# Kernel optimization log

Hardware: AMD Instinct MI355X
Metric: run time of the kernel (lower is better)

Reference implementation:

```python
import jax, jax.numpy as jnp
import numpy as np

B, L, D, H, M = 2, 4096, 1024, 16, 256
DH = D // H
EPS = 1e-6
LN_EPS = 1e-5


def setup_inputs() -> dict:
    key = jax.random.key(0)
    ks = jax.random.split(key, 6)
    inp = {
        "x": jax.random.normal(ks[0], (B, L, D), jnp.float32),
        "Wq": jax.random.normal(ks[1], (D, D), jnp.float32) * (D ** -0.5),
        "Wk": jax.random.normal(ks[2], (D, D), jnp.float32) * (D ** -0.5),
        "Wv": jax.random.normal(ks[3], (D, D), jnp.float32) * (D ** -0.5),
        "Wo": jax.random.normal(ks[4], (D, D), jnp.float32) * (D ** -0.5),
        "proj": jax.random.normal(ks[5], (H, M, DH), jnp.float32),
        "ln_g": jnp.ones((D,), jnp.float32),
        "ln_b": jnp.zeros((D,), jnp.float32),
        "scale_factor": 2,
    }
    return inp


def _heads(t, W):
    b, l, _ = t.shape
    return (t @ W).reshape(b, l, H, DH).transpose(0, 2, 1, 3)  # bhld


def _favor_features(u, proj):
    # u: [B,H,L,DH] already scaled by d_head**-0.25; proj: [H,M,DH]
    dash = jnp.einsum("bhld,hmd->bhlm", u, proj)
    diag = 0.5 * jnp.sum(u * u, axis=-1, keepdims=True)  # [B,H,L,1]
    stab = jnp.max(dash, axis=-1, keepdims=True)
    return jnp.exp(dash - diag - stab) * (M ** -0.5)  # [B,H,L,M]


def reference(x, Wq, Wk, Wv, Wo, proj, ln_g, ln_b, scale_factor):
    b, l, d = x.shape
    # nearest-neighbor upsample along sequence (F.interpolate default mode)
    up = jnp.repeat(x, scale_factor, axis=1)  # [B, L*s, D]

    scale = DH ** -0.25
    q = _heads(up, Wq) * scale   # [B,H,Lq,DH]
    k = _heads(x, Wk) * scale    # [B,H,L,DH]
    v = _heads(x, Wv)            # [B,H,L,DH]

    qf = _favor_features(q, proj)  # [B,H,Lq,M]
    kf = _favor_features(k, proj)  # [B,H,L,M]

    kv = jnp.einsum("bhlm,bhld->bhmd", kf, v)          # [B,H,M,DH]
    k_sum = jnp.sum(kf, axis=2)                          # [B,H,M]
    z = 1.0 / (jnp.einsum("bhlm,bhm->bhl", qf, k_sum) + EPS)
    attn = jnp.einsum("bhlm,bhmd->bhld", qf, kv) * z[..., None]

    lq = attn.shape[2]
    y = attn.transpose(0, 2, 1, 3).reshape(b, lq, d) @ Wo
    y = jax.nn.gelu(y, approximate=False)

    mu = jnp.mean(y, axis=-1, keepdims=True)
    var = jnp.mean((y - mu) ** 2, axis=-1, keepdims=True)
    return (y - mu) * jax.lax.rsqrt(var + LN_EPS) * ln_g + ln_b
```

## Files before the change

### kernel.cpp

```cpp
#include <hip/hip_runtime.h>

static constexpr int kB  = 2;
static constexpr int kL  = 4096;
static constexpr int kD  = 1024;
static constexpr int kH  = 16;
static constexpr int kDH = 64;
static constexpr int kM  = 256;
static constexpr int kN  = kB * kL;
static constexpr float kScale    = 0.35355339059327373f;
static constexpr float kInvSqrtM = 0.0625f;
static constexpr float kEps   = 1e-6f;
static constexpr float kLnEps = 1e-5f;

typedef __attribute__((ext_vector_type(8))) short short8;
typedef __attribute__((ext_vector_type(4))) float f32x4;

__device__ __forceinline__ float bf2f(unsigned short h) {
  union { unsigned int u; float f; } c;
  c.u = ((unsigned int)h) << 16;
  return c.f;
}
__device__ __forceinline__ unsigned short f2bf(float f) {
  union { float f; unsigned int u; } c;
  c.f = f;
  unsigned int u = c.u;
  u += 0x7fffu + ((u >> 16) & 1u);
  return (unsigned short)(u >> 16);
}

__device__ __forceinline__ void gload_lds16(const unsigned short* g,
                                            unsigned short* l) {
  __builtin_amdgcn_global_load_lds(
      (const __attribute__((address_space(1))) unsigned int*)g,
      (__attribute__((address_space(3))) unsigned int*)l, 16, 0, 0);
}

__device__ __forceinline__ void xcd_swizzle(int& bx, int& by) {
  const int nwg = gridDim.x * gridDim.y;
  const int bid = blockIdx.x + gridDim.x * blockIdx.y;
  const int cpx = nwg >> 3;
  const int sb  = (bid & 7) * cpx + (bid >> 3);
  bx = sb % gridDim.x;
  by = sb / gridDim.x;
}

__global__ __launch_bounds__(256) void cast_bf16_kernel(
    const float* __restrict__ in, unsigned short* __restrict__ out)
{
  const int i = blockIdx.x * 256 + threadIdx.x;
  float4 v = ((const float4*)in)[i];
  ushort4 o;
  o.x = f2bf(v.x); o.y = f2bf(v.y); o.z = f2bf(v.z); o.w = f2bf(v.w);
  ((ushort4*)out)[i] = o;
}

__global__ __launch_bounds__(256) void transpose_cast4_kernel(
    const float* __restrict__ W0, const float* __restrict__ W1,
    const float* __restrict__ W2, const float* __restrict__ W3,
    unsigned short* __restrict__ WqkvT, unsigned short* __restrict__ WoT)
{
  __shared__ float tile[32][33];
  const int z = blockIdx.z;
  const float* W = (z == 0) ? W0 : (z == 1) ? W1 : (z == 2) ? W2 : W3;
  unsigned short* WT = (z < 3) ? (WqkvT + (size_t)z * kD * kD) : WoT;
  const int n0 = blockIdx.x * 32, k0 = blockIdx.y * 32;
  const int t = threadIdx.x, kk = t >> 5, nn = t & 31;
#pragma unroll
  for (int i = 0; i < 4; ++i)
    tile[kk + i * 8][nn] = W[(size_t)(k0 + kk + i * 8) * kD + n0 + nn];
  __syncthreads();
#pragma unroll
  for (int i = 0; i < 4; ++i)
    WT[(size_t)(n0 + kk + i * 8) * kD + k0 + nn] = f2bf(tile[nn][kk + i * 8]);
}

__global__ __launch_bounds__(256) void gemm_qk_mfma(
    const unsigned short* __restrict__ A, const unsigned short* __restrict__ BT,
    unsigned short* __restrict__ Qb, unsigned short* __restrict__ Kb)
{
  __shared__ unsigned short As[128 * 32];
  __shared__ unsigned short Bs[128 * 32];
  const int tid = threadIdx.x, lane = tid & 63, w = tid >> 6;
  const int q = lane >> 4, c = lane & 15;
  const int wr = (w >> 1) * 64, wc = (w & 1) * 64;
  int bx, by; xcd_swizzle(bx, by);
  const int row0 = by * 128, col0 = bx * 128;
  const int lrow = lane >> 2, lcol = (lane & 3) * 8;

  f32x4 acc[4][4];
#pragma unroll
  for (int i = 0; i < 4; ++i)
#pragma unroll
    for (int j = 0; j < 4; ++j) acc[i][j] = (f32x4)0.f;

  for (int k0 = 0; k0 < kD; k0 += 32) {
#pragma unroll
    for (int i = 0; i < 2; ++i) {
      const int r0 = w * 32 + i * 16;
      gload_lds16(&A[(size_t)(row0 + r0 + lrow) * kD + k0 + lcol], &As[r0 * 32]);
      gload_lds16(&BT[(size_t)(col0 + r0 + lrow) * kD + k0 + lcol], &Bs[r0 * 32]);
    }
    __syncthreads();
    short8 av[4], bv[4];
#pragma unroll
    for (int i = 0; i < 4; ++i)
      av[i] = *(const short8*)&As[(wr + i * 16 + c) * 32 + q * 8];
#pragma unroll
    for (int j = 0; j < 4; ++j)
      bv[j] = *(const short8*)&Bs[(wc + j * 16 + c) * 32 + q * 8];
#pragma unroll
    for (int i = 0; i < 4; ++i)
#pragma unroll
      for (int j = 0; j < 4; ++j)
        acc[i][j] = __builtin_amdgcn_mfma_f32_16x16x32_bf16(
            av[i], bv[j], acc[i][j], 0, 0, 0);
    __syncthreads();
  }

  unsigned short* O = (col0 < 1024) ? Qb : Kb;
  const int cl0 = col0 & 1023;
#pragma unroll
  for (int i = 0; i < 4; ++i)
#pragma unroll
    for (int j = 0; j < 4; ++j)
#pragma unroll
      for (int r = 0; r < 4; ++r) {
        const int row = row0 + wr + i * 16 + q * 4 + r;
        const int col = cl0 + wc + j * 16 + c;
        O[(size_t)row * kD + col] = f2bf(kScale * acc[i][j][r]);
      }
}

__global__ __launch_bounds__(256) void gemm_vt_mfma(
    const unsigned short* __restrict__ A, const unsigned short* __restrict__ BT,
    unsigned short* __restrict__ VT)
{
  __shared__ unsigned short As[128 * 32];
  __shared__ unsigned short Bs[128 * 32];
  const int tid = threadIdx.x, lane = tid & 63, w = tid >> 6;
  const int q = lane >> 4, c = lane & 15;
  const int wr = (w >> 1) * 64, wc = (w & 1) * 64;
  int bx, by; xcd_swizzle(bx, by);
  const int row0 = bx * 128, col0 = by * 128;
  const int lrow = lane >> 2, lcol = (lane & 3) * 8;

  f32x4 acc[4][4];
#pragma unroll
  for (int i = 0; i < 4; ++i)
#pragma unroll
    for (int j = 0; j < 4; ++j) acc[i][j] = (f32x4)0.f;

  for (int k0 = 0; k0 < kD; k0 += 32) {
#pragma unroll
    for (int i = 0; i < 2; ++i) {
      const int r0 = w * 32 + i * 16;
      gload_lds16(&A[(size_t)(row0 + r0 + lrow) * kD + k0 + lcol], &As[r0 * 32]);
      gload_lds16(&BT[(size_t)(col0 + r0 + lrow) * kD + k0 + lcol], &Bs[r0 * 32]);
    }
    __syncthreads();
    short8 av[4], bv[4];
#pragma unroll
    for (int i = 0; i < 4; ++i)
      av[i] = *(const short8*)&As[(wr + i * 16 + c) * 32 + q * 8];
#pragma unroll
    for (int j = 0; j < 4; ++j)
      bv[j] = *(const short8*)&Bs[(wc + j * 16 + c) * 32 + q * 8];
#pragma unroll
    for (int i = 0; i < 4; ++i)
#pragma unroll
      for (int j = 0; j < 4; ++j)
        acc[i][j] = __builtin_amdgcn_mfma_f32_16x16x32_bf16(
            av[i], bv[j], acc[i][j], 0, 0, 0);
    __syncthreads();
  }

#pragma unroll
  for (int i = 0; i < 4; ++i)
#pragma unroll
    for (int j = 0; j < 4; ++j)
#pragma unroll
      for (int r = 0; r < 4; ++r) {
        const int row = row0 + wr + i * 16 + q * 4 + r;
        const int col = col0 + wc + j * 16 + c;
        const int bq = col >> 12, l = col & 4095;
        const int h = row >> 6, d = row & 63;
        VT[((size_t)((bq * 16 + h) * 64 + d)) * (size_t)kL + l] =
            f2bf(acc[i][j][r]);
      }
}

__global__ __launch_bounds__(256) void gemm_wo_mfma(
    const unsigned short* __restrict__ A, const unsigned short* __restrict__ BT,
    float* __restrict__ Cout)
{
  __shared__ unsigned short As[128 * 32];
  __shared__ unsigned short Bs[128 * 32];
  const int tid = threadIdx.x, lane = tid & 63, w = tid >> 6;
  const int q = lane >> 4, c = lane & 15;
  const int wr = (w >> 1) * 64, wc = (w & 1) * 64;
  int bx, by; xcd_swizzle(bx, by);
  const int row0 = by * 128, col0 = bx * 128;
  const int lrow = lane >> 2, lcol = (lane & 3) * 8;

  f32x4 acc[4][4];
#pragma unroll
  for (int i = 0; i < 4; ++i)
#pragma unroll
    for (int j = 0; j < 4; ++j) acc[i][j] = (f32x4)0.f;

  for (int k0 = 0; k0 < kD; k0 += 32) {
#pragma unroll
    for (int i = 0; i < 2; ++i) {
      const int r0 = w * 32 + i * 16;
      gload_lds16(&A[(size_t)(row0 + r0 + lrow) * kD + k0 + lcol], &As[r0 * 32]);
      gload_lds16(&BT[(size_t)(col0 + r0 + lrow) * kD + k0 + lcol], &Bs[r0 * 32]);
    }
    __syncthreads();
    short8 av[4], bv[4];
#pragma unroll
    for (int i = 0; i < 4; ++i)
      av[i] = *(const short8*)&As[(wr + i * 16 + c) * 32 + q * 8];
#pragma unroll
    for (int j = 0; j < 4; ++j)
      bv[j] = *(const short8*)&Bs[(wc + j * 16 + c) * 32 + q * 8];
#pragma unroll
    for (int i = 0; i < 4; ++i)
#pragma unroll
      for (int j = 0; j < 4; ++j)
        acc[i][j] = __builtin_amdgcn_mfma_f32_16x16x32_bf16(
            av[i], bv[j], acc[i][j], 0, 0, 0);
    __syncthreads();
  }

#pragma unroll
  for (int i = 0; i < 4; ++i)
#pragma unroll
    for (int j = 0; j < 4; ++j)
#pragma unroll
      for (int r = 0; r < 4; ++r) {
        const int row = row0 + wr + i * 16 + q * 4 + r;
        const int col = col0 + wc + j * 16 + c;
        Cout[(size_t)row * kD + col] = acc[i][j][r];
      }
}

template <int TRANS>
__global__ __launch_bounds__(256) void favor_mfma(
    const unsigned short* __restrict__ U, const unsigned short* __restrict__ projb,
    unsigned short* __restrict__ F)
{
  __shared__ unsigned short Us[128 * 72];
  __shared__ unsigned short Ps[256 * 72];
  __shared__ float diagp[256];
  __shared__ float diag[128];
  unsigned short* Tbuf = Us;
  const int bh = blockIdx.x, b = bh >> 4, h = bh & 15;
  const int l0 = blockIdx.y * 128;
  const int tid = threadIdx.x, lane = tid & 63, w = tid >> 6;
  const int q = lane >> 4, c = lane & 15;
  const int wr = w * 32;

#pragma unroll
  for (int it = 0; it < 4; ++it) {
    int idx = it * 256 + tid;
    int row = idx >> 3, col8 = idx & 7;
    *(uint4*)&Us[row * 72 + col8 * 8] =
        *(const uint4*)&U[((size_t)(b * kL + l0 + row)) * kD + h * kDH + col8 * 8];
  }
#pragma unroll
  for (int it = 0; it < 8; ++it) {
    int idx = it * 256 + tid;
    int row = idx >> 3, col8 = idx & 7;
    *(uint4*)&Ps[row * 72 + col8 * 8] =
        *(const uint4*)&projb[((size_t)(h * kM + row)) * kDH + col8 * 8];
  }
  __syncthreads();

  {
    int row = tid & 127, half = tid >> 7;
    const unsigned short* ur = &Us[row * 72 + half * 32];
    float s = 0.f;
#pragma unroll
    for (int d8 = 0; d8 < 4; ++d8) {
      uint4 raw = *(const uint4*)&ur[d8 * 8];
      const unsigned short* us = (const unsigned short*)&raw;
#pragma unroll
      for (int j = 0; j < 8; ++j) { float v = bf2f(us[j]); s = fmaf(v, v, s); }
    }
    diagp[half * 128 + row] = s;
  }

  f32x4 acc[2][16];
#pragma unroll
  for (int i = 0; i < 2; ++i)
#pragma unroll
    for (int j = 0; j < 16; ++j) acc[i][j] = (f32x4)0.f;

#pragma unroll
  for (int ks = 0; ks < 2; ++ks) {
    short8 av[2];
#pragma unroll
    for (int i = 0; i < 2; ++i)
      av[i] = *(const short8*)&Us[(wr + i * 16 + c) * 72 + ks * 32 + q * 8];
#pragma unroll
    for (int jb = 0; jb < 2; ++jb) {
      short8 bv[8];
#pragma unroll
      for (int jl = 0; jl < 8; ++jl)
        bv[jl] = *(const short8*)&Ps[((jb * 8 + jl) * 16 + c) * 72 + ks * 32 + q * 8];
#pragma unroll
      for (int jl = 0; jl < 8; ++jl)
#pragma unroll
        for (int i = 0; i < 2; ++i)
          acc[i][jb * 8 + jl] = __builtin_amdgcn_mfma_f32_16x16x32_bf16(
              av[i], bv[jl], acc[i][jb * 8 + jl], 0, 0, 0);
    }
  }

  __syncthreads();
  if (tid < 128) diag[tid] = 0.5f * (diagp[tid] + diagp[128 + tid]);
  __syncthreads();

#pragma unroll
  for (int i = 0; i < 2; ++i)
#pragma unroll
    for (int r = 0; r < 4; ++r) {
      const int lrow = wr + i * 16 + q * 4 + r;
      float mx = -3.4e38f;
#pragma unroll
      for (int j = 0; j < 16; ++j) mx = fmaxf(mx, acc[i][j][r]);
      mx = fmaxf(mx, __shfl_xor(mx, 1, 64));
      mx = fmaxf(mx, __shfl_xor(mx, 2, 64));
      mx = fmaxf(mx, __shfl_xor(mx, 4, 64));
      mx = fmaxf(mx, __shfl_xor(mx, 8, 64));
      const float base = diag[lrow] + mx;
      if (TRANS == 0) {
        const size_t gbase = ((size_t)bh * kL + (l0 + lrow)) * kM;
#pragma unroll
        for (int j = 0; j < 16; ++j)
          F[gbase + j * 16 + c] = f2bf(__expf(acc[i][j][r] - base) * kInvSqrtM);
      } else {
#pragma unroll
        for (int j = 0; j < 16; ++j)
          acc[i][j][r] = __expf(acc[i][j][r] - base) * kInvSqrtM;
      }
    }

  if (TRANS == 1) {
#pragma unroll
    for (int mc = 0; mc < 4; ++mc) {
      __syncthreads();
#pragma unroll
      for (int jl = 0; jl < 4; ++jl) {
        const int jj = mc * 4 + jl;
#pragma unroll
        for (int i = 0; i < 2; ++i) {
          ushort4 o;
          o.x = f2bf(acc[i][jj][0]); o.y = f2bf(acc[i][jj][1]);
          o.z = f2bf(acc[i][jj][2]); o.w = f2bf(acc[i][jj][3]);
          *(ushort4*)&Tbuf[(jl * 16 + c) * 136 + wr + i * 16 + q * 4] = o;
        }
      }
      __syncthreads();
#pragma unroll
      for (int it = 0; it < 4; ++it) {
        int idx = it * 256 + tid;
        int row = idx >> 4, col8 = idx & 15;
        *(uint4*)&F[((size_t)(bh * kM + mc * 64 + row)) * (size_t)kL +
                    l0 + col8 * 8] = *(const uint4*)&Tbuf[row * 136 + col8 * 8];
      }
    }
  }
}

__global__ __launch_bounds__(256) void kv_mfma(
    const unsigned short* __restrict__ KFT, const unsigned short* __restrict__ VT,
    float* __restrict__ KVP, float* __restrict__ KSP)
{
  __shared__ unsigned short As[128 * 32];
  __shared__ unsigned short Bs[64 * 32];
  const int bh = blockIdx.x, mtile = blockIdx.y, split = blockIdx.z;
  const int tid = threadIdx.x, lane = tid & 63, w = tid >> 6;
  const int q = lane >> 4, c = lane & 15;
  const int l0 = split * 512;
  const unsigned short* Abase = KFT + ((size_t)(bh * kM + mtile * 128)) * kL + l0;
  const unsigned short* Bbase = VT + ((size_t)(bh * kDH)) * kL + l0;
  const int lrow = lane >> 2, lcol = (lane & 3) * 8;

  f32x4 acc[2][4];
#pragma unroll
  for (int i = 0; i < 2; ++i)
#pragma unroll
    for (int j = 0; j < 4; ++j) acc[i][j] = (f32x4)0.f;
  float ksr[2] = {0.f, 0.f};

  for (int k0 = 0; k0 < 512; k0 += 32) {
#pragma unroll
    for (int i = 0; i < 2; ++i) {
      const int r0 = w * 32 + i * 16;
      gload_lds16(&Abase[(size_t)(r0 + lrow) * kL + k0 + lcol], &As[r0 * 32]);
    }
    gload_lds16(&Bbase[(size_t)(w * 16 + lrow) * kL + k0 + lcol], &Bs[w * 16 * 32]);
    __syncthreads();
    short8 av[2], bv[4];
#pragma unroll
    for (int i = 0; i < 2; ++i) {
      av[i] = *(const short8*)&As[(w * 32 + i * 16 + c) * 32 + q * 8];
#pragma unroll
      for (int e = 0; e < 8; ++e) ksr[i] += bf2f((unsigned short)av[i][e]);
    }
#pragma unroll
    for (int j = 0; j < 4; ++j)
      bv[j] = *(const short8*)&Bs[(j * 16 + c) * 32 + q * 8];
#pragma unroll
    for (int i = 0; i < 2; ++i)
#pragma unroll
      for (int j = 0; j < 4; ++j)
        acc[i][j] = __builtin_amdgcn_mfma_f32_16x16x32_bf16(
            av[i], bv[j], acc[i][j], 0, 0, 0);
    __syncthreads();
  }

  const int blk = (bh * 2 + mtile) * 8 + split;
  float* op = KVP + (size_t)blk * (128 * 64);
#pragma unroll
  for (int i = 0; i < 2; ++i)
#pragma unroll
    for (int j = 0; j < 4; ++j)
#pragma unroll
      for (int r = 0; r < 4; ++r)
        op[(w * 32 + i * 16 + q * 4 + r) * 64 + j * 16 + c] = acc[i][j][r];

#pragma unroll
  for (int i = 0; i < 2; ++i) {
    float s = ksr[i];
    s += __shfl_xor(s, 16, 64);
    s += __shfl_xor(s, 32, 64);
    if (q == 0) KSP[blk * 128 + w * 32 + i * 16 + c] = s;
  }
}

__global__ __launch_bounds__(256) void kv_reduce_kernel(
    const float* __restrict__ KVP, const float* __restrict__ KSP,
    unsigned short* __restrict__ KVT)
{
  const int blk = blockIdx.x;
  const int bh = blk / 80, n = blk - bh * 80;
  const int t = threadIdx.x;
  const int mt = t >> 7, ml = t & 127;
  float s = 0.f;
  if (n < 64) {
#pragma unroll
    for (int sp = 0; sp < 8; ++sp)
      s += KVP[((size_t)((bh * 2 + mt) * 8 + sp)) * (128 * 64) + ml * 64 + n];
  } else if (n == 64) {
#pragma unroll
    for (int sp = 0; sp < 8; ++sp)
      s += KSP[((bh * 2 + mt) * 8 + sp) * 128 + ml];
  }
  KVT[(size_t)bh * (80 * kM) + n * kM + t] = f2bf(s);
}

__global__ __launch_bounds__(256) void attn_mfma(
    const unsigned short* __restrict__ QF, const unsigned short* __restrict__ KVT,
    unsigned short* __restrict__ ATTN)
{
  __shared__ unsigned short kvs[80 * 264];
  __shared__ unsigned short qs[128 * 40];
  const int bh = blockIdx.x, b = bh >> 4, h = bh & 15;
  const int l0 = blockIdx.y * 128;
  const int tid = threadIdx.x, lane = tid & 63, w = tid >> 6;
  const int q = lane >> 4, c = lane & 15;
  const int trow = tid >> 2, tc8 = (tid & 3) * 8;

#pragma unroll
  for (int it = 0; it < 20; ++it) {
    int idx4 = it * 256 + tid;
    int row = idx4 >> 6, col4 = idx4 & 63;
    *(ushort4*)&kvs[row * 264 + col4 * 4] =
        *(const ushort4*)&KVT[(size_t)bh * (80 * kM) + row * kM + col4 * 4];
  }

  f32x4 acc[2][5];
#pragma unroll
  for (int i = 0; i < 2; ++i)
#pragma unroll
    for (int j = 0; j < 5; ++j) acc[i][j] = (f32x4)0.f;

  for (int kk = 0; kk < 8; ++kk) {
    __syncthreads();
#pragma unroll
    for (int i = 0; i < 2; ++i)
      *(uint4*)&qs[(trow + 64 * i) * 40 + tc8] =
          *(const uint4*)&QF[((size_t)bh * kL + (l0 + trow + 64 * i)) * kM +
                             kk * 32 + tc8];
    __syncthreads();
    short8 bv[5];
#pragma unroll
    for (int j = 0; j < 5; ++j)
      bv[j] = *(const short8*)&kvs[(j * 16 + c) * 264 + kk * 32 + q * 8];
#pragma unroll
    for (int i = 0; i < 2; ++i) {
      short8 av = *(const short8*)&qs[(w * 32 + i * 16 + c) * 40 + q * 8];
#pragma unroll
      for (int j = 0; j < 5; ++j)
        acc[i][j] = __builtin_amdgcn_mfma_f32_16x16x32_bf16(
            av, bv[j], acc[i][j], 0, 0, 0);
    }
  }

#pragma unroll
  for (int i = 0; i < 2; ++i)
#pragma unroll
    for (int r = 0; r < 4; ++r) {
      float den = __shfl(acc[i][4][r], (lane & 48));
      float z = 1.f / (den + kEps);
      const int row = l0 + w * 32 + i * 16 + q * 4 + r;
      const size_t base = ((size_t)(b * kL + row)) * kD + h * kDH;
#pragma unroll
      for (int j = 0; j < 4; ++j)
        ATTN[base + j * 16 + c] = f2bf(acc[i][j][r] * z);
    }
}

__global__ __launch_bounds__(256) void gelu_ln_kernel(
    const float* __restrict__ Y, const float* __restrict__ lng,
    const float* __restrict__ lnb, float* __restrict__ OUT)
{
  __shared__ float r1[4], r2[4];
  const int n = blockIdx.x;
  const int tid = threadIdx.x, lane = tid & 63, w = tid >> 6;

  float4 y4 = ((const float4*)(Y + (size_t)n * kD))[tid];
  float g0 = 0.5f * y4.x * (1.f + erff(y4.x * 0.70710678118654752f));
  float g1 = 0.5f * y4.y * (1.f + erff(y4.y * 0.70710678118654752f));
  float g2 = 0.5f * y4.z * (1.f + erff(y4.z * 0.70710678118654752f));
  float g3 = 0.5f * y4.w * (1.f + erff(y4.w * 0.70710678118654752f));

  float s  = (g0 + g1) + (g2 + g3);
  float ss = (g0 * g0 + g1 * g1) + (g2 * g2 + g3 * g3);
#pragma unroll
  for (int off = 32; off; off >>= 1) {
    s  += __shfl_xor(s, off, 64);
    ss += __shfl_xor(ss, off, 64);
  }
  if (lane == 0) { r1[w] = s; r2[w] = ss; }
  __syncthreads();
  s  = (r1[0] + r1[1]) + (r1[2] + r1[3]);
  ss = (r2[0] + r2[1]) + (r2[2] + r2[3]);
  float mu  = s * (1.f / (float)kD);
  float var = ss * (1.f / (float)kD) - mu * mu;
  float inv = rsqrtf(var + kLnEps);

  float4 gg = ((const float4*)lng)[tid];
  float4 bb = ((const float4*)lnb)[tid];
  float4 o;
  o.x = (g0 - mu) * inv * gg.x + bb.x;
  o.y = (g1 - mu) * inv * gg.y + bb.y;
  o.z = (g2 - mu) * inv * gg.z + bb.z;
  o.w = (g3 - mu) * inv * gg.w + bb.w;

  const int b = n >> 12, l = n & 4095;
  const int cc = tid * 4;
  size_t base = ((size_t)(b * 8192 + 2 * l)) * kD + cc;
  *(float4*)(OUT + base)      = o;
  *(float4*)(OUT + base + kD) = o;
}

extern "C" void kernel_launch(void* const* d_in, const int* in_sizes, int n_in,
                              void* d_out, int out_size, void* d_ws, size_t ws_size,
                              hipStream_t stream)
{
  (void)in_sizes; (void)n_in; (void)out_size; (void)ws_size;
  const float* x    = (const float*)d_in[0];
  const float* Wq   = (const float*)d_in[1];
  const float* Wk   = (const float*)d_in[2];
  const float* Wv   = (const float*)d_in[3];
  const float* Wo   = (const float*)d_in[4];
  const float* proj = (const float*)d_in[5];
  const float* lng  = (const float*)d_in[6];
  const float* lnb  = (const float*)d_in[7];
  float* out = (float*)d_out;

  char* ws = (char*)d_ws;
  const size_t MB = 1024 * 1024;
  unsigned short* xb    = (unsigned short*)(ws);
  unsigned short* WqkvT = (unsigned short*)(ws + 16 * MB);
  unsigned short* WoT   = (unsigned short*)(ws + 22 * MB);
  unsigned short* Qb    = (unsigned short*)(ws + 24 * MB);
  unsigned short* Kb    = (unsigned short*)(ws + 40 * MB);
  unsigned short* VT    = (unsigned short*)(ws + 56 * MB);
  unsigned short* QF    = (unsigned short*)(ws + 72 * MB);
  unsigned short* KFT   = (unsigned short*)(ws + 136 * MB);
  float* KSP            = (float*)(ws + 200 * MB);
  unsigned short* KVT   = (unsigned short*)(ws + 201 * MB);
  unsigned short* projb = (unsigned short*)(ws + 203 * MB);
  float* KVP            = (float*)(ws + 24 * MB);
  unsigned short* ATTN  = Kb;
  float* Y              = (float*)(ws + 72 * MB);
  unsigned short* WvT   = WqkvT + (size_t)2 * kD * kD;

  cast_bf16_kernel<<<(kN * kD) / 1024, 256, 0, stream>>>(x, xb);
  cast_bf16_kernel<<<(kH * kM * kDH) / 1024, 256, 0, stream>>>(proj, projb);
  transpose_cast4_kernel<<<dim3(32, 32, 4), 256, 0, stream>>>(
      Wq, Wk, Wv, Wo, WqkvT, WoT);

  gemm_qk_mfma<<<dim3(16, 64), 256, 0, stream>>>(xb, WqkvT, Qb, Kb);
  gemm_vt_mfma<<<dim3(8, 64), 256, 0, stream>>>(WvT, xb, VT);

  favor_mfma<0><<<dim3(32, 32), 256, 0, stream>>>(Qb, projb, QF);
  favor_mfma<1><<<dim3(32, 32), 256, 0, stream>>>(Kb, projb, KFT);

  kv_mfma<<<dim3(32, 2, 8), 256, 0, stream>>>(KFT, VT, KVP, KSP);
  kv_reduce_kernel<<<32 * 80, 256, 0, stream>>>(KVP, KSP, KVT);

  attn_mfma<<<dim3(32, 32), 256, 0, stream>>>(QF, KVT, ATTN);

  gemm_wo_mfma<<<dim3(8, 64), 256, 0, stream>>>(ATTN, WoT, Y);

  gelu_ln_kernel<<<kN, 256, 0, stream>>>(Y, lng, lnb, out);
}
```

Baseline: 352.7 us.

## Double-buffer LDS tiles in GEMM and KV kernels; store Wo output as bf16

```diff
diff --git a/kernel.cpp b/kernel.cpp
--- a/kernel.cpp
+++ b/kernel.cpp
@@ -78,8 +78,8 @@
     const unsigned short* __restrict__ A, const unsigned short* __restrict__ BT,
     unsigned short* __restrict__ Qb, unsigned short* __restrict__ Kb)
 {
-  __shared__ unsigned short As[128 * 32];
-  __shared__ unsigned short Bs[128 * 32];
+  __shared__ unsigned short As[2][128 * 32];
+  __shared__ unsigned short Bs[2][128 * 32];
   const int tid = threadIdx.x, lane = tid & 63, w = tid >> 6;
   const int q = lane >> 4, c = lane & 15;
   const int wr = (w >> 1) * 64, wc = (w & 1) * 64;
@@ -93,28 +93,40 @@
 #pragma unroll
     for (int j = 0; j < 4; ++j) acc[i][j] = (f32x4)0.f;
 
+#pragma unroll
+  for (int i = 0; i < 2; ++i) {
+    const int r0 = w * 32 + i * 16;
+    gload_lds16(&A[(size_t)(row0 + r0 + lrow) * kD + lcol], &As[0][r0 * 32]);
+    gload_lds16(&BT[(size_t)(col0 + r0 + lrow) * kD + lcol], &Bs[0][r0 * 32]);
+  }
+
+  int cur = 0;
   for (int k0 = 0; k0 < kD; k0 += 32) {
-#pragma unroll
-    for (int i = 0; i < 2; ++i) {
-      const int r0 = w * 32 + i * 16;
-      gload_lds16(&A[(size_t)(row0 + r0 + lrow) * kD + k0 + lcol], &As[r0 * 32]);
-      gload_lds16(&BT[(size_t)(col0 + r0 + lrow) * kD + k0 + lcol], &Bs[r0 * 32]);
-    }
     __syncthreads();
+    if (k0 + 32 < kD) {
+#pragma unroll
+      for (int i = 0; i < 2; ++i) {
+        const int r0 = w * 32 + i * 16;
+        gload_lds16(&A[(size_t)(row0 + r0 + lrow) * kD + k0 + 32 + lcol],
+                    &As[cur ^ 1][r0 * 32]);
+        gload_lds16(&BT[(size_t)(col0 + r0 + lrow) * kD + k0 + 32 + lcol],
+                    &Bs[cur ^ 1][r0 * 32]);
+      }
+    }
     short8 av[4], bv[4];
 #pragma unroll
     for (int i = 0; i < 4; ++i)
-      av[i] = *(const short8*)&As[(wr + i * 16 + c) * 32 + q * 8];
-#pragma unroll
-    for (int j = 0; j < 4; ++j)
-      bv[j] = *(const short8*)&Bs[(wc + j * 16 + c) * 32 + q * 8];
+      av[i] = *(const short8*)&As[cur][(wr + i * 16 + c) * 32 + q * 8];
+#pragma unroll
+    for (int j = 0; j < 4; ++j)
+      bv[j] = *(const short8*)&Bs[cur][(wc + j * 16 + c) * 32 + q * 8];
 #pragma unroll
     for (int i = 0; i < 4; ++i)
 #pragma unroll
       for (int j = 0; j < 4; ++j)
         acc[i][j] = __builtin_amdgcn_mfma_f32_16x16x32_bf16(
             av[i], bv[j], acc[i][j], 0, 0, 0);
-    __syncthreads();
+    cur ^= 1;
   }
 
   unsigned short* O = (col0 < 1024) ? Qb : Kb;
@@ -135,8 +147,8 @@
     const unsigned short* __restrict__ A, const unsigned short* __restrict__ BT,
     unsigned short* __restrict__ VT)
 {
-  __shared__ unsigned short As[128 * 32];
-  __shared__ unsigned short Bs[128 * 32];
+  __shared__ unsigned short As[2][128 * 32];
+  __shared__ unsigned short Bs[2][128 * 32];
   const int tid = threadIdx.x, lane = tid & 63, w = tid >> 6;
   const int q = lane >> 4, c = lane & 15;
   const int wr = (w >> 1) * 64, wc = (w & 1) * 64;
@@ -150,28 +162,40 @@
 #pragma unroll
     for (int j = 0; j < 4; ++j) acc[i][j] = (f32x4)0.f;
 
+#pragma unroll
+  for (int i = 0; i < 2; ++i) {
+    const int r0 = w * 32 + i * 16;
+    gload_lds16(&A[(size_t)(row0 + r0 + lrow) * kD + lcol], &As[0][r0 * 32]);
+    gload_lds16(&BT[(size_t)(col0 + r0 + lrow) * kD + lcol], &Bs[0][r0 * 32]);
+  }
+
+  int cur = 0;
   for (int k0 = 0; k0 < kD; k0 += 32) {
-#pragma unroll
-    for (int i = 0; i < 2; ++i) {
-      const int r0 = w * 32 + i * 16;
-      gload_lds16(&A[(size_t)(row0 + r0 + lrow) * kD + k0 + lcol], &As[r0 * 32]);
-      gload_lds16(&BT[(size_t)(col0 + r0 + lrow) * kD + k0 + lcol], &Bs[r0 * 32]);
-    }
     __syncthreads();
+    if (k0 + 32 < kD) {
+#pragma unroll
+      for (int i = 0; i < 2; ++i) {
+        const int r0 = w * 32 + i * 16;
+        gload_lds16(&A[(size_t)(row0 + r0 + lrow) * kD + k0 + 32 + lcol],
+                    &As[cur ^ 1][r0 * 32]);
+        gload_lds16(&BT[(size_t)(col0 + r0 + lrow) * kD + k0 + 32 + lcol],
+                    &Bs[cur ^ 1][r0 * 32]);
+      }
+    }
     short8 av[4], bv[4];
 #pragma unroll
     for (int i = 0; i < 4; ++i)
-      av[i] = *(const short8*)&As[(wr + i * 16 + c) * 32 + q * 8];
-#pragma unroll
-    for (int j = 0; j < 4; ++j)
-      bv[j] = *(const short8*)&Bs[(wc + j * 16 + c) * 32 + q * 8];
+      av[i] = *(const short8*)&As[cur][(wr + i * 16 + c) * 32 + q * 8];
+#pragma unroll
+    for (int j = 0; j < 4; ++j)
+      bv[j] = *(const short8*)&Bs[cur][(wc + j * 16 + c) * 32 + q * 8];
 #pragma unroll
     for (int i = 0; i < 4; ++i)
 #pragma unroll
       for (int j = 0; j < 4; ++j)
         acc[i][j] = __builtin_amdgcn_mfma_f32_16x16x32_bf16(
             av[i], bv[j], acc[i][j], 0, 0, 0);
-    __syncthreads();
+    cur ^= 1;
   }
 
 #pragma unroll
@@ -191,10 +215,10 @@
 
 __global__ __launch_bounds__(256) void gemm_wo_mfma(
     const unsigned short* __restrict__ A, const unsigned short* __restrict__ BT,
-    float* __restrict__ Cout)
-{
-  __shared__ unsigned short As[128 * 32];
-  __shared__ unsigned short Bs[128 * 32];
+    unsigned short* __restrict__ Yb)
+{
+  __shared__ unsigned short As[2][128 * 32];
+  __shared__ unsigned short Bs[2][128 * 32];
   const int tid = threadIdx.x, lane = tid & 63, w = tid >> 6;
   const int q = lane >> 4, c = lane & 15;
   const int wr = (w >> 1) * 64, wc = (w & 1) * 64;
@@ -208,28 +232,40 @@
 #pragma unroll
     for (int j = 0; j < 4; ++j) acc[i][j] = (f32x4)0.f;
 
+#pragma unroll
+  for (int i = 0; i < 2; ++i) {
+    const int r0 = w * 32 + i * 16;
+    gload_lds16(&A[(size_t)(row0 + r0 + lrow) * kD + lcol], &As[0][r0 * 32]);
+    gload_lds16(&BT[(size_t)(col0 + r0 + lrow) * kD + lcol], &Bs[0][r0 * 32]);
+  }
+
+  int cur = 0;
   for (int k0 = 0; k0 < kD; k0 += 32) {
-#pragma unroll
-    for (int i = 0; i < 2; ++i) {
-      const int r0 = w * 32 + i * 16;
-      gload_lds16(&A[(size_t)(row0 + r0 + lrow) * kD + k0 + lcol], &As[r0 * 32]);
-      gload_lds16(&BT[(size_t)(col0 + r0 + lrow) * kD + k0 + lcol], &Bs[r0 * 32]);
-    }
     __syncthreads();
+    if (k0 + 32 < kD) {
+#pragma unroll
+      for (int i = 0; i < 2; ++i) {
+        const int r0 = w * 32 + i * 16;
+        gload_lds16(&A[(size_t)(row0 + r0 + lrow) * kD + k0 + 32 + lcol],
+                    &As[cur ^ 1][r0 * 32]);
+        gload_lds16(&BT[(size_t)(col0 + r0 + lrow) * kD + k0 + 32 + lcol],
+                    &Bs[cur ^ 1][r0 * 32]);
+      }
+    }
     short8 av[4], bv[4];
 #pragma unroll
     for (int i = 0; i < 4; ++i)
-      av[i] = *(const short8*)&As[(wr + i * 16 + c) * 32 + q * 8];
-#pragma unroll
-    for (int j = 0; j < 4; ++j)
-      bv[j] = *(const short8*)&Bs[(wc + j * 16 + c) * 32 + q * 8];
+      av[i] = *(const short8*)&As[cur][(wr + i * 16 + c) * 32 + q * 8];
+#pragma unroll
+    for (int j = 0; j < 4; ++j)
+      bv[j] = *(const short8*)&Bs[cur][(wc + j * 16 + c) * 32 + q * 8];
 #pragma unroll
     for (int i = 0; i < 4; ++i)
 #pragma unroll
       for (int j = 0; j < 4; ++j)
         acc[i][j] = __builtin_amdgcn_mfma_f32_16x16x32_bf16(
             av[i], bv[j], acc[i][j], 0, 0, 0);
-    __syncthreads();
+    cur ^= 1;
   }
 
 #pragma unroll
@@ -240,7 +276,7 @@
       for (int r = 0; r < 4; ++r) {
         const int row = row0 + wr + i * 16 + q * 4 + r;
         const int col = col0 + wc + j * 16 + c;
-        Cout[(size_t)row * kD + col] = acc[i][j][r];
+        Yb[(size_t)row * kD + col] = f2bf(acc[i][j][r]);
       }
 }
 
@@ -377,8 +413,8 @@
     const unsigned short* __restrict__ KFT, const unsigned short* __restrict__ VT,
     float* __restrict__ KVP, float* __restrict__ KSP)
 {
-  __shared__ unsigned short As[128 * 32];
-  __shared__ unsigned short Bs[64 * 32];
+  __shared__ unsigned short As[2][128 * 32];
+  __shared__ unsigned short Bs[2][64 * 32];
   const int bh = blockIdx.x, mtile = blockIdx.y, split = blockIdx.z;
   const int tid = threadIdx.x, lane = tid & 63, w = tid >> 6;
   const int q = lane >> 4, c = lane & 15;
@@ -394,31 +430,43 @@
     for (int j = 0; j < 4; ++j) acc[i][j] = (f32x4)0.f;
   float ksr[2] = {0.f, 0.f};
 
+#pragma unroll
+  for (int i = 0; i < 2; ++i) {
+    const int r0 = w * 32 + i * 16;
+    gload_lds16(&Abase[(size_t)(r0 + lrow) * kL + lcol], &As[0][r0 * 32]);
+  }
+  gload_lds16(&Bbase[(size_t)(w * 16 + lrow) * kL + lcol], &Bs[0][w * 16 * 32]);
+
+  int cur = 0;
   for (int k0 = 0; k0 < 512; k0 += 32) {
+    __syncthreads();
+    if (k0 + 32 < 512) {
+#pragma unroll
+      for (int i = 0; i < 2; ++i) {
+        const int r0 = w * 32 + i * 16;
+        gload_lds16(&Abase[(size_t)(r0 + lrow) * kL + k0 + 32 + lcol],
+                    &As[cur ^ 1][r0 * 32]);
+      }
+      gload_lds16(&Bbase[(size_t)(w * 16 + lrow) * kL + k0 + 32 + lcol],
+                  &Bs[cur ^ 1][w * 16 * 32]);
+    }
+    short8 av[2], bv[4];
 #pragma unroll
     for (int i = 0; i < 2; ++i) {
-      const int r0 = w * 32 + i * 16;
-      gload_lds16(&Abase[(size_t)(r0 + lrow) * kL + k0 + lcol], &As[r0 * 32]);
-    }
-    gload_lds16(&Bbase[(size_t)(w * 16 + lrow) * kL + k0 + lcol], &Bs[w * 16 * 32]);
-    __syncthreads();
-    short8 av[2], bv[4];
-#pragma unroll
-    for (int i = 0; i < 2; ++i) {
-      av[i] = *(const short8*)&As[(w * 32 + i * 16 + c) * 32 + q * 8];
+      av[i] = *(const short8*)&As[cur][(w * 32 + i * 16 + c) * 32 + q * 8];
 #pragma unroll
       for (int e = 0; e < 8; ++e) ksr[i] += bf2f((unsigned short)av[i][e]);
     }
 #pragma unroll
     for (int j = 0; j < 4; ++j)
-      bv[j] = *(const short8*)&Bs[(j * 16 + c) * 32 + q * 8];
+      bv[j] = *(const short8*)&Bs[cur][(j * 16 + c) * 32 + q * 8];
 #pragma unroll
     for (int i = 0; i < 2; ++i)
 #pragma unroll
       for (int j = 0; j < 4; ++j)
         acc[i][j] = __builtin_amdgcn_mfma_f32_16x16x32_bf16(
             av[i], bv[j], acc[i][j], 0, 0, 0);
-    __syncthreads();
+    cur ^= 1;
   }
 
   const int blk = (bh * 2 + mtile) * 8 + split;
@@ -524,18 +572,19 @@
 }
 
 __global__ __launch_bounds__(256) void gelu_ln_kernel(
-    const float* __restrict__ Y, const float* __restrict__ lng,
+    const unsigned short* __restrict__ Yb, const float* __restrict__ lng,
     const float* __restrict__ lnb, float* __restrict__ OUT)
 {
   __shared__ float r1[4], r2[4];
   const int n = blockIdx.x;
   const int tid = threadIdx.x, lane = tid & 63, w = tid >> 6;
 
-  float4 y4 = ((const float4*)(Y + (size_t)n * kD))[tid];
-  float g0 = 0.5f * y4.x * (1.f + erff(y4.x * 0.70710678118654752f));
-  float g1 = 0.5f * y4.y * (1.f + erff(y4.y * 0.70710678118654752f));
-  float g2 = 0.5f * y4.z * (1.f + erff(y4.z * 0.70710678118654752f));
-  float g3 = 0.5f * y4.w * (1.f + erff(y4.w * 0.70710678118654752f));
+  ushort4 yv = ((const ushort4*)(Yb + (size_t)n * kD))[tid];
+  float y0 = bf2f(yv.x), y1 = bf2f(yv.y), y2 = bf2f(yv.z), y3 = bf2f(yv.w);
+  float g0 = 0.5f * y0 * (1.f + erff(y0 * 0.70710678118654752f));
+  float g1 = 0.5f * y1 * (1.f + erff(y1 * 0.70710678118654752f));
+  float g2 = 0.5f * y2 * (1.f + erff(y2 * 0.70710678118654752f));
+  float g3 = 0.5f * y3 * (1.f + erff(y3 * 0.70710678118654752f));
 
   float s  = (g0 + g1) + (g2 + g3);
   float ss = (g0 * g0 + g1 * g1) + (g2 * g2 + g3 * g3);
@@ -597,7 +646,7 @@
   unsigned short* projb = (unsigned short*)(ws + 203 * MB);
   float* KVP            = (float*)(ws + 24 * MB);
   unsigned short* ATTN  = Kb;
-  float* Y              = (float*)(ws + 72 * MB);
+  unsigned short* Yb    = QF;
   unsigned short* WvT   = WqkvT + (size_t)2 * kD * kD;
 
   cast_bf16_kernel<<<(kN * kD) / 1024, 256, 0, stream>>>(x, xb);
@@ -616,7 +665,7 @@
 
   attn_mfma<<<dim3(32, 32), 256, 0, stream>>>(QF, KVT, ATTN);
 
-  gemm_wo_mfma<<<dim3(8, 64), 256, 0, stream>>>(ATTN, WoT, Y);
-
-  gelu_ln_kernel<<<kN, 256, 0, stream>>>(Y, lng, lnb, out);
-}
+  gemm_wo_mfma<<<dim3(8, 64), 256, 0, stream>>>(ATTN, WoT, Yb);
+
+  gelu_ln_kernel<<<kN, 256, 0, stream>>>(Yb, lng, lnb, out);
+}
```

Result: no change. 357.4 us (+1.3%).

## Fuse query FAVOR feature computation into attention kernel and store Wo output as bf16

Applied to the files above, without the earlier changes.

```diff
diff --git a/kernel.cpp b/kernel.cpp
--- a/kernel.cpp
+++ b/kernel.cpp
@@ -191,7 +191,7 @@
 
 __global__ __launch_bounds__(256) void gemm_wo_mfma(
     const unsigned short* __restrict__ A, const unsigned short* __restrict__ BT,
-    float* __restrict__ Cout)
+    unsigned short* __restrict__ Yb)
 {
   __shared__ unsigned short As[128 * 32];
   __shared__ unsigned short Bs[128 * 32];
@@ -240,12 +240,11 @@
       for (int r = 0; r < 4; ++r) {
         const int row = row0 + wr + i * 16 + q * 4 + r;
         const int col = col0 + wc + j * 16 + c;
-        Cout[(size_t)row * kD + col] = acc[i][j][r];
+        Yb[(size_t)row * kD + col] = f2bf(acc[i][j][r]);
       }
 }
 
-template <int TRANS>
-__global__ __launch_bounds__(256) void favor_mfma(
+__global__ __launch_bounds__(256) void favor_k_mfma(
     const unsigned short* __restrict__ U, const unsigned short* __restrict__ projb,
     unsigned short* __restrict__ F)
 {
@@ -334,43 +333,185 @@
       mx = fmaxf(mx, __shfl_xor(mx, 4, 64));
       mx = fmaxf(mx, __shfl_xor(mx, 8, 64));
       const float base = diag[lrow] + mx;
-      if (TRANS == 0) {
-        const size_t gbase = ((size_t)bh * kL + (l0 + lrow)) * kM;
-#pragma unroll
-        for (int j = 0; j < 16; ++j)
-          F[gbase + j * 16 + c] = f2bf(__expf(acc[i][j][r] - base) * kInvSqrtM);
-      } else {
-#pragma unroll
-        for (int j = 0; j < 16; ++j)
-          acc[i][j][r] = __expf(acc[i][j][r] - base) * kInvSqrtM;
+#pragma unroll
+      for (int j = 0; j < 16; ++j)
+        acc[i][j][r] = __expf(acc[i][j][r] - base) * kInvSqrtM;
+    }
+
+#pragma unroll
+  for (int mc = 0; mc < 4; ++mc) {
+    __syncthreads();
+#pragma unroll
+    for (int jl = 0; jl < 4; ++jl) {
+      const int jj = mc * 4 + jl;
+#pragma unroll
+      for (int i = 0; i < 2; ++i) {
+        ushort4 o;
+        o.x = f2bf(acc[i][jj][0]); o.y = f2bf(acc[i][jj][1]);
+        o.z = f2bf(acc[i][jj][2]); o.w = f2bf(acc[i][jj][3]);
+        *(ushort4*)&Tbuf[(jl * 16 + c) * 136 + wr + i * 16 + q * 4] = o;
       }
     }
-
-  if (TRANS == 1) {
-#pragma unroll
-    for (int mc = 0; mc < 4; ++mc) {
-      __syncthreads();
-#pragma unroll
-      for (int jl = 0; jl < 4; ++jl) {
-        const int jj = mc * 4 + jl;
-#pragma unroll
-        for (int i = 0; i < 2; ++i) {
-          ushort4 o;
-          o.x = f2bf(acc[i][jj][0]); o.y = f2bf(acc[i][jj][1]);
-          o.z = f2bf(acc[i][jj][2]); o.w = f2bf(acc[i][jj][3]);
-          *(ushort4*)&Tbuf[(jl * 16 + c) * 136 + wr + i * 16 + q * 4] = o;
-        }
+    __syncthreads();
+#pragma unroll
+    for (int it = 0; it < 4; ++it) {
+      int idx = it * 256 + tid;
+      int row = idx >> 4, col8 = idx & 15;
+      *(uint4*)&F[((size_t)(bh * kM + mc * 64 + row)) * (size_t)kL +
+                  l0 + col8 * 8] = *(const uint4*)&Tbuf[row * 136 + col8 * 8];
+    }
+  }
+}
+
+__global__ __launch_bounds__(256) void fused_qf_attn(
+    const unsigned short* __restrict__ U, const unsigned short* __restrict__ projb,
+    const unsigned short* __restrict__ KVT, unsigned short* __restrict__ ATTN)
+{
+  __shared__ unsigned short SA[27648];
+  __shared__ float diagp[256];
+  __shared__ float diag[128];
+  unsigned short* Us  = SA;
+  unsigned short* Ps  = SA + 9216;
+  unsigned short* kvs = SA;
+  unsigned short* qs  = SA + 21120;
+  const int bh = blockIdx.x, b = bh >> 4, h = bh & 15;
+  const int l0 = blockIdx.y * 128;
+  const int tid = threadIdx.x, lane = tid & 63, w = tid >> 6;
+  const int q = lane >> 4, c = lane & 15;
+  const int wr = w * 32;
+
+#pragma unroll
+  for (int it = 0; it < 4; ++it) {
+    int idx = it * 256 + tid;
+    int row = idx >> 3, col8 = idx & 7;
+    *(uint4*)&Us[row * 72 + col8 * 8] =
+        *(const uint4*)&U[((size_t)(b * kL + l0 + row)) * kD + h * kDH + col8 * 8];
+  }
+#pragma unroll
+  for (int it = 0; it < 8; ++it) {
+    int idx = it * 256 + tid;
+    int row = idx >> 3, col8 = idx & 7;
+    *(uint4*)&Ps[row * 72 + col8 * 8] =
+        *(const uint4*)&projb[((size_t)(h * kM + row)) * kDH + col8 * 8];
+  }
+  __syncthreads();
+
+  {
+    int row = tid & 127, half = tid >> 7;
+    const unsigned short* ur = &Us[row * 72 + half * 32];
+    float s = 0.f;
+#pragma unroll
+    for (int d8 = 0; d8 < 4; ++d8) {
+      uint4 raw = *(const uint4*)&ur[d8 * 8];
+      const unsigned short* us = (const unsigned short*)&raw;
+#pragma unroll
+      for (int j = 0; j < 8; ++j) { float v = bf2f(us[j]); s = fmaf(v, v, s); }
+    }
+    diagp[half * 128 + row] = s;
+  }
+
+  f32x4 acc[2][16];
+#pragma unroll
+  for (int i = 0; i < 2; ++i)
+#pragma unroll
+    for (int j = 0; j < 16; ++j) acc[i][j] = (f32x4)0.f;
+
+#pragma unroll
+  for (int ks = 0; ks < 2; ++ks) {
+    short8 av[2];
+#pragma unroll
+    for (int i = 0; i < 2; ++i)
+      av[i] = *(const short8*)&Us[(wr + i * 16 + c) * 72 + ks * 32 + q * 8];
+#pragma unroll
+    for (int jb = 0; jb < 2; ++jb) {
+      short8 bv[8];
+#pragma unroll
+      for (int jl = 0; jl < 8; ++jl)
+        bv[jl] = *(const short8*)&Ps[((jb * 8 + jl) * 16 + c) * 72 + ks * 32 + q * 8];
+#pragma unroll
+      for (int jl = 0; jl < 8; ++jl)
+#pragma unroll
+        for (int i = 0; i < 2; ++i)
+          acc[i][jb * 8 + jl] = __builtin_amdgcn_mfma_f32_16x16x32_bf16(
+              av[i], bv[jl], acc[i][jb * 8 + jl], 0, 0, 0);
+    }
+  }
+
+  __syncthreads();
+  if (tid < 128) diag[tid] = 0.5f * (diagp[tid] + diagp[128 + tid]);
+#pragma unroll
+  for (int it = 0; it < 10; ++it) {
+    int idx = it * 256 + tid;
+    int row = idx >> 5, col8 = (idx & 31) * 8;
+    *(uint4*)&kvs[row * 264 + col8] =
+        *(const uint4*)&KVT[(size_t)bh * (80 * kM) + row * kM + col8];
+  }
+  __syncthreads();
+
+#pragma unroll
+  for (int i = 0; i < 2; ++i)
+#pragma unroll
+    for (int r = 0; r < 4; ++r) {
+      const int lrow = wr + i * 16 + q * 4 + r;
+      float mx = -3.4e38f;
+#pragma unroll
+      for (int j = 0; j < 16; ++j) mx = fmaxf(mx, acc[i][j][r]);
+      mx = fmaxf(mx, __shfl_xor(mx, 1, 64));
+      mx = fmaxf(mx, __shfl_xor(mx, 2, 64));
+      mx = fmaxf(mx, __shfl_xor(mx, 4, 64));
+      mx = fmaxf(mx, __shfl_xor(mx, 8, 64));
+      const float base = diag[lrow] + mx;
+#pragma unroll
+      for (int j = 0; j < 16; ++j)
+        acc[i][j][r] = __expf(acc[i][j][r] - base) * kInvSqrtM;
+    }
+
+  f32x4 acc2[2][5];
+#pragma unroll
+  for (int i = 0; i < 2; ++i)
+#pragma unroll
+    for (int j = 0; j < 5; ++j) acc2[i][j] = (f32x4)0.f;
+
+#pragma unroll
+  for (int kk = 0; kk < 8; ++kk) {
+#pragma unroll
+    for (int i = 0; i < 2; ++i)
+#pragma unroll
+      for (int jj2 = 0; jj2 < 2; ++jj2) {
+        const int jj = kk * 2 + jj2;
+#pragma unroll
+        for (int r = 0; r < 4; ++r)
+          qs[(wr + i * 16 + q * 4 + r) * 40 + jj2 * 16 + c] =
+              f2bf(acc[i][jj][r]);
       }
-      __syncthreads();
-#pragma unroll
-      for (int it = 0; it < 4; ++it) {
-        int idx = it * 256 + tid;
-        int row = idx >> 4, col8 = idx & 15;
-        *(uint4*)&F[((size_t)(bh * kM + mc * 64 + row)) * (size_t)kL +
-                    l0 + col8 * 8] = *(const uint4*)&Tbuf[row * 136 + col8 * 8];
-      }
-    }
-  }
+    __syncthreads();
+    short8 bv2[5];
+#pragma unroll
+    for (int j = 0; j < 5; ++j)
+      bv2[j] = *(const short8*)&kvs[(j * 16 + c) * 264 + kk * 32 + q * 8];
+#pragma unroll
+    for (int i = 0; i < 2; ++i) {
+      short8 av2 = *(const short8*)&qs[(w * 32 + i * 16 + c) * 40 + q * 8];
+#pragma unroll
+      for (int j = 0; j < 5; ++j)
+        acc2[i][j] = __builtin_amdgcn_mfma_f32_16x16x32_bf16(
+            av2, bv2[j], acc2[i][j], 0, 0, 0);
+    }
+    __syncthreads();
+  }
+
+#pragma unroll
+  for (int i = 0; i < 2; ++i)
+#pragma unroll
+    for (int r = 0; r < 4; ++r) {
+      float den = __shfl(acc2[i][4][r], (lane & 48));
+      float z = 1.f / (den + kEps);
+      const int row = l0 + w * 32 + i * 16 + q * 4 + r;
+      const size_t base = ((size_t)(b * kL + row)) * kD + h * kDH;
+#pragma unroll
+      for (int j = 0; j < 4; ++j)
+        ATTN[base + j * 16 + c] = f2bf(acc2[i][j][r] * z);
+    }
 }
 
 __global__ __launch_bounds__(256) void kv_mfma(
@@ -461,81 +602,20 @@
   KVT[(size_t)bh * (80 * kM) + n * kM + t] = f2bf(s);
 }
 
-__global__ __launch_bounds__(256) void attn_mfma(
-    const unsigned short* __restrict__ QF, const unsigned short* __restrict__ KVT,
-    unsigned short* __restrict__ ATTN)
-{
-  __shared__ unsigned short kvs[80 * 264];
-  __shared__ unsigned short qs[128 * 40];
-  const int bh = blockIdx.x, b = bh >> 4, h = bh & 15;
-  const int l0 = blockIdx.y * 128;
-  const int tid = threadIdx.x, lane = tid & 63, w = tid >> 6;
-  const int q = lane >> 4, c = lane & 15;
-  const int trow = tid >> 2, tc8 = (tid & 3) * 8;
-
-#pragma unroll
-  for (int it = 0; it < 20; ++it) {
-    int idx4 = it * 256 + tid;
-    int row = idx4 >> 6, col4 = idx4 & 63;
-    *(ushort4*)&kvs[row * 264 + col4 * 4] =
-        *(const ushort4*)&KVT[(size_t)bh * (80 * kM) + row * kM + col4 * 4];
-  }
-
-  f32x4 acc[2][5];
-#pragma unroll
-  for (int i = 0; i < 2; ++i)
-#pragma unroll
-    for (int j = 0; j < 5; ++j) acc[i][j] = (f32x4)0.f;
-
-  for (int kk = 0; kk < 8; ++kk) {
-    __syncthreads();
-#pragma unroll
-    for (int i = 0; i < 2; ++i)
-      *(uint4*)&qs[(trow + 64 * i) * 40 + tc8] =
-          *(const uint4*)&QF[((size_t)bh * kL + (l0 + trow + 64 * i)) * kM +
-                             kk * 32 + tc8];
-    __syncthreads();
-    short8 bv[5];
-#pragma unroll
-    for (int j = 0; j < 5; ++j)
-      bv[j] = *(const short8*)&kvs[(j * 16 + c) * 264 + kk * 32 + q * 8];
-#pragma unroll
-    for (int i = 0; i < 2; ++i) {
-      short8 av = *(const short8*)&qs[(w * 32 + i * 16 + c) * 40 + q * 8];
-#pragma unroll
-      for (int j = 0; j < 5; ++j)
-        acc[i][j] = __builtin_amdgcn_mfma_f32_16x16x32_bf16(
-            av, bv[j], acc[i][j], 0, 0, 0);
-    }
-  }
-
-#pragma unroll
-  for (int i = 0; i < 2; ++i)
-#pragma unroll
-    for (int r = 0; r < 4; ++r) {
-      float den = __shfl(acc[i][4][r], (lane & 48));
-      float z = 1.f / (den + kEps);
-      const int row = l0 + w * 32 + i * 16 + q * 4 + r;
-      const size_t base = ((size_t)(b * kL + row)) * kD + h * kDH;
-#pragma unroll
-      for (int j = 0; j < 4; ++j)
-        ATTN[base + j * 16 + c] = f2bf(acc[i][j][r] * z);
-    }
-}
-
 __global__ __launch_bounds__(256) void gelu_ln_kernel(
-    const float* __restrict__ Y, const float* __restrict__ lng,
+    const unsigned short* __restrict__ Yb, const float* __restrict__ lng,
     const float* __restrict__ lnb, float* __restrict__ OUT)
 {
   __shared__ float r1[4], r2[4];
   const int n = blockIdx.x;
   const int tid = threadIdx.x, lane = tid & 63, w = tid >> 6;
 
-  float4 y4 = ((const float4*)(Y + (size_t)n * kD))[tid];
-  float g0 = 0.5f * y4.x * (1.f + erff(y4.x * 0.70710678118654752f));
-  float g1 = 0.5f * y4.y * (1.f + erff(y4.y * 0.70710678118654752f));
-  float g2 = 0.5f * y4.z * (1.f + erff(y4.z * 0.70710678118654752f));
-  float g3 = 0.5f * y4.w * (1.f + erff(y4.w * 0.70710678118654752f));
+  ushort4 yv = ((const ushort4*)(Yb + (size_t)n * kD))[tid];
+  float y0 = bf2f(yv.x), y1 = bf2f(yv.y), y2 = bf2f(yv.z), y3 = bf2f(yv.w);
+  float g0 = 0.5f * y0 * (1.f + erff(y0 * 0.70710678118654752f));
+  float g1 = 0.5f * y1 * (1.f + erff(y1 * 0.70710678118654752f));
+  float g2 = 0.5f * y2 * (1.f + erff(y2 * 0.70710678118654752f));
+  float g3 = 0.5f * y3 * (1.f + erff(y3 * 0.70710678118654752f));
 
   float s  = (g0 + g1) + (g2 + g3);
   float ss = (g0 * g0 + g1 * g1) + (g2 * g2 + g3 * g3);
@@ -590,14 +670,13 @@
   unsigned short* Qb    = (unsigned short*)(ws + 24 * MB);
   unsigned short* Kb    = (unsigned short*)(ws + 40 * MB);
   unsigned short* VT    = (unsigned short*)(ws + 56 * MB);
-  unsigned short* QF    = (unsigned short*)(ws + 72 * MB);
+  float* KVP            = (float*)(ws + 72 * MB);
   unsigned short* KFT   = (unsigned short*)(ws + 136 * MB);
   float* KSP            = (float*)(ws + 200 * MB);
   unsigned short* KVT   = (unsigned short*)(ws + 201 * MB);
   unsigned short* projb = (unsigned short*)(ws + 203 * MB);
-  float* KVP            = (float*)(ws + 24 * MB);
   unsigned short* ATTN  = Kb;
-  float* Y              = (float*)(ws + 72 * MB);
+  unsigned short* Yb    = (unsigned short*)(ws + 72 * MB);
   unsigned short* WvT   = WqkvT + (size_t)2 * kD * kD;
 
   cast_bf16_kernel<<<(kN * kD) / 1024, 256, 0, stream>>>(x, xb);
@@ -608,15 +687,13 @@
   gemm_qk_mfma<<<dim3(16, 64), 256, 0, stream>>>(xb, WqkvT, Qb, Kb);
   gemm_vt_mfma<<<dim3(8, 64), 256, 0, stream>>>(WvT, xb, VT);
 
-  favor_mfma<0><<<dim3(32, 32), 256, 0, stream>>>(Qb, projb, QF);
-  favor_mfma<1><<<dim3(32, 32), 256, 0, stream>>>(Kb, projb, KFT);
-
+  favor_k_mfma<<<dim3(32, 32), 256, 0, stream>>>(Kb, projb, KFT);
   kv_mfma<<<dim3(32, 2, 8), 256, 0, stream>>>(KFT, VT, KVP, KSP);
   kv_reduce_kernel<<<32 * 80, 256, 0, stream>>>(KVP, KSP, KVT);
 
-  attn_mfma<<<dim3(32, 32), 256, 0, stream>>>(QF, KVT, ATTN);
-
-  gemm_wo_mfma<<<dim3(8, 64), 256, 0, stream>>>(ATTN, WoT, Y);
-
-  gelu_ln_kernel<<<kN, 256, 0, stream>>>(Y, lng, lnb, out);
-}
+  fused_qf_attn<<<dim3(32, 32), 256, 0, stream>>>(Qb, projb, KVT, ATTN);
+
+  gemm_wo_mfma<<<dim3(8, 64), 256, 0, stream>>>(ATTN, WoT, Yb);
+
+  gelu_ln_kernel<<<kN, 256, 0, stream>>>(Yb, lng, lnb, out);
+}
```

New measurement: 336.3 us. 1.05x faster.
